# Performance work log

Measured on AMD Instinct MI355X. Metric: run time of the kernel, lower is better.

## Reference

```python
import jax, jax.numpy as jnp
import numpy as np

EPS = 1e-6

def _rmsnorm(x, w):
    var = jnp.mean(x * x, axis=-1, keepdims=True)
    return x * jax.lax.rsqrt(var + EPS) * w

def setup_inputs() -> dict:
    key = jax.random.key(0)
    ks = jax.random.split(key, 10)
    B, S, D = 2, 2048, 1024
    H, E, F = 16, 8, 4096
    std = 0.02
    return {
        "x": jax.random.normal(ks[0], (B, S, D), dtype=jnp.float32),
        "ln1_w": jnp.ones((D,), dtype=jnp.float32),
        "ln2_w": jnp.ones((D,), dtype=jnp.float32),
        "wq": jax.random.normal(ks[1], (D, D), dtype=jnp.float32) * std,
        "wk": jax.random.normal(ks[2], (D, D), dtype=jnp.float32) * std,
        "wv": jax.random.normal(ks[3], (D, D), dtype=jnp.float32) * std,
        "wo": jax.random.normal(ks[4], (D, D), dtype=jnp.float32) * std,
        "wr": jax.random.normal(ks[5], (D, E), dtype=jnp.float32) * std,
        "w1": jax.random.normal(ks[6], (E, D, F), dtype=jnp.float32) * std,
        "w2": jax.random.normal(ks[7], (E, F, D), dtype=jnp.float32) * std,
    }

def reference(x, ln1_w, ln2_w, wq, wk, wv, wo, wr, w1, w2):
    B, S, D = x.shape
    H = 16
    Dh = D // H
    E = wr.shape[1]
    K = 2
    Z_COEF = 0.001

    # --- bidirectional attention sublayer ---
    residual = x
    xn = _rmsnorm(x, ln1_w)
    q = (xn @ wq).reshape(B, S, H, Dh).transpose(0, 2, 1, 3)  # [B,H,S,Dh]
    k = (xn @ wk).reshape(B, S, H, Dh).transpose(0, 2, 1, 3)
    v = (xn @ wv).reshape(B, S, H, Dh).transpose(0, 2, 1, 3)
    scale = 1.0 / jnp.sqrt(jnp.asarray(Dh, dtype=x.dtype))
    scores = jnp.einsum("bhqd,bhkd->bhqk", q, k) * scale  # non-causal
    attn = jax.nn.softmax(scores, axis=-1)
    ctx = jnp.einsum("bhqk,bhkd->bhqd", attn, v)
    attn_out = ctx.transpose(0, 2, 1, 3).reshape(B, S, D) @ wo
    x = residual + attn_out

    # --- MoE sublayer ---
    residual = x
    xn2 = _rmsnorm(x, ln2_w)
    logits = xn2 @ wr                       # [B,S,E]
    probs = jax.nn.softmax(logits, axis=-1)
    topv, topi = jax.lax.top_k(probs, K)    # [B,S,K]
    weights = topv / jnp.sum(topv, axis=-1, keepdims=True)
    onehot = jax.nn.one_hot(topi, E, dtype=x.dtype)          # [B,S,K,E]
    dispatch = jnp.sum(onehot * weights[..., None], axis=-2)  # [B,S,E] combine weights

    # router losses: switch-style load balance + z-loss
    frac_tokens = jnp.mean(jnp.sum(onehot, axis=-2), axis=(0, 1))  # [E]
    frac_probs = jnp.mean(probs, axis=(0, 1))                      # [E]
    aux_loss = E * jnp.sum(frac_tokens * frac_probs) / K
    z = jax.nn.logsumexp(logits, axis=-1)
    router_loss = aux_loss + Z_COEF * jnp.mean(z * z)

    # expert-grouped FFN: dense per expert, masked combine (loop over fixed E)
    expert_out = jnp.zeros_like(xn2)
    for e in range(E):
        h = jax.nn.gelu(xn2 @ w1[e])
        expert_out = expert_out + dispatch[..., e:e + 1] * (h @ w2[e])

    out = residual + expert_out
    return out, router_loss
```

## Files before the change

### kernel.cpp

```cpp
#include <hip/hip_runtime.h>
#include <hip/hip_bf16.h>
#include <math.h>

#define DEV static __device__ __forceinline__

typedef __attribute__((ext_vector_type(8))) short short8;
typedef __attribute__((ext_vector_type(8))) unsigned short ushort8;
typedef __attribute__((ext_vector_type(4))) unsigned short ushort4v;
typedef __attribute__((ext_vector_type(4))) float floatx4;

using bf16 = __hip_bfloat16;

constexpr int Bc = 2, Sc = 2048, Dc = 1024, Hc = 16, DHc = 64, Ec = 8, Fc = 4096;
constexpr int Tc = Bc * Sc;

DEV float b2f(unsigned short u) {
  union { unsigned int i; float f; } c; c.i = ((unsigned int)u) << 16; return c.f;
}
DEV unsigned short f2b(float f) {
  bf16 h = __float2bfloat16(f);
  return *(unsigned short*)&h;
}

DEV floatx4 mfma_bf16(short8 a, short8 b, floatx4 c) {
  return __builtin_amdgcn_mfma_f32_16x16x32_bf16(a, b, c, 0, 0, 0);
}

DEV float gelu_tanh(float x) {
  float z = 0.7978845608028654f * (x + 0.044715f * x * x * x);
  z = fminf(fmaxf(z, -15.f), 15.f);
  float t = __expf(2.f * z);
  return 0.5f * x * (1.f + (t - 1.f) / (t + 1.f));
}

DEV void gemm_core(bf16* As, bf16* Bs,
                   const bf16* __restrict__ A, int lda, int Mvalid, int m0,
                   const float* __restrict__ Bm, int N, int Kdim, int n0,
                   floatx4 (&acc)[4][4]) {
  const int tid = threadIdx.x;
  const int lane = tid & 63;
  const int wave = tid >> 6;
  const int wm = wave & 1, wn = wave >> 1;
  const int l15 = lane & 15, quad = lane >> 4;
  (void)lane;

#pragma unroll
  for (int mi = 0; mi < 4; mi++)
#pragma unroll
    for (int ni = 0; ni < 4; ni++)
#pragma unroll
      for (int r = 0; r < 4; r++) acc[mi][ni][r] = 0.f;

  const int nK = Kdim >> 6;
  for (int kb = 0; kb < nK; kb++) {
    const int k0 = kb << 6;
    __syncthreads();
#pragma unroll
    for (int it = 0; it < 4; it++) {
      int c = tid + it * 256;
      int row = c >> 3, kc = (c & 7) << 3;
      short8 v;
      if (m0 + row < Mvalid) {
        v = *(const short8*)(A + (size_t)(m0 + row) * lda + k0 + kc);
      } else {
#pragma unroll
        for (int j = 0; j < 8; j++) v[j] = 0;
      }
      *(short8*)(As + row * 72 + kc) = v;
    }
#pragma unroll
    for (int it = 0; it < 2; it++) {
      int u = tid + it * 256;
      int kp = u >> 4, cg = u & 15;
      const float* bp = Bm + (size_t)(k0 + 2 * kp) * N + n0 + cg * 8;
      floatx4 r0a = *(const floatx4*)bp;
      floatx4 r0b = *(const floatx4*)(bp + 4);
      floatx4 r1a = *(const floatx4*)(bp + N);
      floatx4 r1b = *(const floatx4*)(bp + N + 4);
#pragma unroll
      for (int j = 0; j < 8; j++) {
        float v0 = (j < 4) ? r0a[j] : r0b[j - 4];
        float v1 = (j < 4) ? r1a[j] : r1b[j - 4];
        int col = cg * 8 + j;
        int elem = col * 72 + ((((kp >> 2) ^ (col >> 3)) & 7) << 3) + ((kp & 3) << 1);
        *(unsigned int*)(Bs + elem) = (unsigned int)f2b(v0) | ((unsigned int)f2b(v1) << 16);
      }
    }
    __syncthreads();
#pragma unroll
    for (int kk = 0; kk < 64; kk += 32) {
      const int gbase = (kk >> 3) & 4;
      short8 af[4], bfr[4];
#pragma unroll
      for (int mi = 0; mi < 4; mi++)
        af[mi] = *(const short8*)(As + (wm * 64 + mi * 16 + l15) * 72 + kk + quad * 8);
#pragma unroll
      for (int ni = 0; ni < 4; ni++) {
        int col = wn * 64 + ni * 16 + l15;
        int g = quad + gbase;
        bfr[ni] = *(const short8*)(Bs + col * 72 + (((g ^ (col >> 3)) & 7) << 3));
      }
#pragma unroll
      for (int mi = 0; mi < 4; mi++)
#pragma unroll
        for (int ni = 0; ni < 4; ni++)
          acc[mi][ni] = mfma_bf16(af[mi], bfr[ni], acc[mi][ni]);
    }
  }
}

#define GEMM_SHARED \
  __shared__ __align__(16) bf16 As[128 * 72]; \
  __shared__ __align__(16) bf16 Bs[128 * 72];
#define LANE_DECODE \
  const int tid = threadIdx.x; const int lane = tid & 63; const int wave = tid >> 6; \
  const int wm = wave & 1, wn = wave >> 1; const int l15 = lane & 15, quad = lane >> 4; \
  (void)tid; (void)lane;

__global__ __launch_bounds__(256) void k_rms(const float* __restrict__ x,
                                             const float* __restrict__ w,
                                             bf16* __restrict__ out,
                                             float* __restrict__ outf) {
  __shared__ float red[4];
  const int tid = threadIdx.x, lane = tid & 63, wave = tid >> 6;
  const size_t base = (size_t)blockIdx.x * Dc + tid * 4;
  floatx4 v = *(const floatx4*)(x + base);
  float ss = v[0] * v[0] + v[1] * v[1] + v[2] * v[2] + v[3] * v[3];
#pragma unroll
  for (int off = 32; off >= 1; off >>= 1) ss += __shfl_xor(ss, off);
  if (lane == 0) red[wave] = ss;
  __syncthreads();
  float tot = red[0] + red[1] + red[2] + red[3];
  float rr = rsqrtf(tot * (1.f / Dc) + 1e-6f);
  floatx4 wv = *(const floatx4*)(w + tid * 4);
  floatx4 res;
#pragma unroll
  for (int j = 0; j < 4; j++) res[j] = v[j] * rr * wv[j];
#pragma unroll
  for (int j = 0; j < 4; j++) out[base + j] = __float2bfloat16(res[j]);
  if (outf) *(floatx4*)(outf + base) = res;
}

__global__ __launch_bounds__(256) void k_gemm_qkv(
    const bf16* __restrict__ xn, const float* __restrict__ wq,
    const float* __restrict__ wk, const float* __restrict__ wv,
    bf16* __restrict__ q, bf16* __restrict__ k, bf16* __restrict__ v) {
  GEMM_SHARED; LANE_DECODE;
  const float* W = blockIdx.z == 0 ? wq : (blockIdx.z == 1 ? wk : wv);
  bf16* out = blockIdx.z == 0 ? q : (blockIdx.z == 1 ? k : v);
  const int m0 = blockIdx.y * 128, n0 = blockIdx.x * 128;
  floatx4 acc[4][4];
  gemm_core(As, Bs, xn, Dc, Tc, m0, W, Dc, Dc, n0, acc);
#pragma unroll
  for (int mi = 0; mi < 4; mi++)
#pragma unroll
    for (int ni = 0; ni < 4; ni++)
#pragma unroll
      for (int r = 0; r < 4; r++) {
        int row = m0 + wm * 64 + mi * 16 + quad * 4 + r;
        int col = n0 + wn * 64 + ni * 16 + l15;
        int b = row >> 11, s = row & 2047, h = col >> 6, dh = col & 63;
        out[((((size_t)b * Hc + h) * Sc + s) << 6) + dh] = __float2bfloat16(acc[mi][ni][r]);
      }
}

__global__ __launch_bounds__(256) void k_gemm_wo(
    const bf16* __restrict__ ctx, const float* __restrict__ wo,
    const float* __restrict__ x, float* __restrict__ x1) {
  GEMM_SHARED; LANE_DECODE;
  const int m0 = blockIdx.y * 128, n0 = blockIdx.x * 128;
  floatx4 acc[4][4];
  gemm_core(As, Bs, ctx, Dc, Tc, m0, wo, Dc, Dc, n0, acc);
#pragma unroll
  for (int mi = 0; mi < 4; mi++)
#pragma unroll
    for (int ni = 0; ni < 4; ni++)
#pragma unroll
      for (int r = 0; r < 4; r++) {
        int row = m0 + wm * 64 + mi * 16 + quad * 4 + r;
        int col = n0 + wn * 64 + ni * 16 + l15;
        size_t idx = (size_t)row * Dc + col;
        x1[idx] = acc[mi][ni][r] + x[idx];
      }
}

__global__ __launch_bounds__(256) void k_attn(
    const bf16* __restrict__ Q, const bf16* __restrict__ K,
    const bf16* __restrict__ V, bf16* __restrict__ ctx) {
  __shared__ __align__(16) bf16 Ks[32 * 72];
  __shared__ __align__(16) bf16 Vs[64 * 40];
  __shared__ __align__(16) bf16 Ps[4 * 16 * 40];
  const int tid = threadIdx.x, lane = tid & 63, wave = tid >> 6;
  const int l15 = lane & 15, quad = lane >> 4;
  const int bh = blockIdx.y;
  const size_t base = (size_t)bh * Sc * DHc;
  const bf16* Qb = Q + base; const bf16* Kb = K + base; const bf16* Vb = V + base;
  const int q0 = blockIdx.x * 64 + wave * 16;
  bf16* Pw = Ps + wave * (16 * 40);

  short8 aq[2];
#pragma unroll
  for (int kk2 = 0; kk2 < 2; kk2++)
    aq[kk2] = *(const short8*)(Qb + (size_t)(q0 + l15) * 64 + kk2 * 32 + quad * 8);

  float m_i[4], l_i[4];
  floatx4 o[4];
#pragma unroll
  for (int r = 0; r < 4; r++) { m_i[r] = -__builtin_inff(); l_i[r] = 0.f; }
#pragma unroll
  for (int n4 = 0; n4 < 4; n4++)
#pragma unroll
    for (int r = 0; r < 4; r++) o[n4][r] = 0.f;

  for (int kt = 0; kt < Sc / 32; kt++) {
    const int kb = kt * 32;
    __syncthreads();
    {
      int row = tid >> 3, kc = (tid & 7) << 3;
      *(short8*)(Ks + row * 72 + kc) = *(const short8*)(Kb + (size_t)(kb + row) * 64 + kc);
    }
    if (tid < 128) {
      int kp = tid >> 3, dg = tid & 7;
      ushort8 a0 = *(const ushort8*)(Vb + (size_t)(kb + 2 * kp) * 64 + dg * 8);
      ushort8 a1 = *(const ushort8*)(Vb + (size_t)(kb + 2 * kp + 1) * 64 + dg * 8);
#pragma unroll
      for (int j = 0; j < 8; j++) {
        int dh = dg * 8 + j;
        int elem = dh * 40 + ((((kp >> 2) ^ (dh >> 3)) & 3) << 3) + ((kp & 3) << 1);
        *(unsigned int*)(Vs + elem) = (unsigned int)a0[j] | ((unsigned int)a1[j] << 16);
      }
    }
    __syncthreads();
    floatx4 sc[2];
#pragma unroll
    for (int ni = 0; ni < 2; ni++) {
#pragma unroll
      for (int r = 0; r < 4; r++) sc[ni][r] = 0.f;
#pragma unroll
      for (int kk2 = 0; kk2 < 2; kk2++) {
        short8 bk = *(const short8*)(Ks + (ni * 16 + l15) * 72 + kk2 * 32 + quad * 8);
        sc[ni] = mfma_bf16(aq[kk2], bk, sc[ni]);
      }
    }
#pragma unroll
    for (int ni = 0; ni < 2; ni++)
#pragma unroll
      for (int r = 0; r < 4; r++) sc[ni][r] *= 0.125f;
    float rmax[4];
#pragma unroll
    for (int r = 0; r < 4; r++) rmax[r] = fmaxf(sc[0][r], sc[1][r]);
#pragma unroll
    for (int off = 1; off < 16; off <<= 1)
#pragma unroll
      for (int r = 0; r < 4; r++) rmax[r] = fmaxf(rmax[r], __shfl_xor(rmax[r], off));
    float alpha[4], rsum[4];
#pragma unroll
    for (int r = 0; r < 4; r++) {
      float nm = fmaxf(m_i[r], rmax[r]);
      alpha[r] = __expf(m_i[r] - nm);
      m_i[r] = nm;
    }
#pragma unroll
    for (int ni = 0; ni < 2; ni++)
#pragma unroll
      for (int r = 0; r < 4; r++) sc[ni][r] = __expf(sc[ni][r] - m_i[r]);
#pragma unroll
    for (int r = 0; r < 4; r++) rsum[r] = sc[0][r] + sc[1][r];
#pragma unroll
    for (int off = 1; off < 16; off <<= 1)
#pragma unroll
      for (int r = 0; r < 4; r++) rsum[r] += __shfl_xor(rsum[r], off);
#pragma unroll
    for (int r = 0; r < 4; r++) l_i[r] = l_i[r] * alpha[r] + rsum[r];
#pragma unroll
    for (int n4 = 0; n4 < 4; n4++)
#pragma unroll
      for (int r = 0; r < 4; r++) o[n4][r] *= alpha[r];
#pragma unroll
    for (int ni = 0; ni < 2; ni++)
#pragma unroll
      for (int r = 0; r < 4; r++)
        Pw[(quad * 4 + r) * 40 + ni * 16 + l15] = __float2bfloat16(sc[ni][r]);
    __syncthreads();
    short8 ap = *(const short8*)(Pw + l15 * 40 + quad * 8);
#pragma unroll
    for (int n4 = 0; n4 < 4; n4++) {
      int dh = n4 * 16 + l15;
      short8 bv = *(const short8*)(Vs + dh * 40 + (((quad ^ (dh >> 3)) & 3) << 3));
      o[n4] = mfma_bf16(ap, bv, o[n4]);
    }
  }
  const int b = bh >> 4, h = bh & 15;
#pragma unroll
  for (int n4 = 0; n4 < 4; n4++)
#pragma unroll
    for (int r = 0; r < 4; r++) {
      int s = q0 + quad * 4 + r;
      int d = h * 64 + n4 * 16 + l15;
      ctx[(size_t)(b * Sc + s) * Dc + d] = __float2bfloat16(o[n4][r] / l_i[r]);
    }
}

__global__ __launch_bounds__(256) void k_router(
    const float* __restrict__ xn2f, const float* __restrict__ wr,
    int* __restrict__ topi, float* __restrict__ topw,
    int* __restrict__ counts, float* __restrict__ sum_probs,
    float* __restrict__ sum_z2) {
  __shared__ float sp[8]; __shared__ float sz[1]; __shared__ int scnt[8];
  const int tid = threadIdx.x, wave = tid >> 6, lane = tid & 63;
  if (tid < 8) { sp[tid] = 0.f; scnt[tid] = 0; }
  if (tid == 0) sz[0] = 0.f;
  __syncthreads();
  const int t = blockIdx.x * 4 + wave;
  float a[8];
#pragma unroll
  for (int e = 0; e < 8; e++) a[e] = 0.f;
  const float* xr = xn2f + (size_t)t * Dc;
#pragma unroll 4
  for (int i = 0; i < 16; i++) {
    int d = lane + i * 64;
    float xv = xr[d];
    floatx4 wa = *(const floatx4*)(wr + d * 8);
    floatx4 wb = *(const floatx4*)(wr + d * 8 + 4);
#pragma unroll
    for (int e = 0; e < 4; e++) a[e] += xv * wa[e];
#pragma unroll
    for (int e = 0; e < 4; e++) a[e + 4] += xv * wb[e];
  }
#pragma unroll
  for (int off = 1; off < 64; off <<= 1)
#pragma unroll
    for (int e = 0; e < 8; e++) a[e] += __shfl_xor(a[e], off);
  float mx = a[0];
#pragma unroll
  for (int e = 1; e < 8; e++) mx = fmaxf(mx, a[e]);
  float pr[8], sum = 0.f;
#pragma unroll
  for (int e = 0; e < 8; e++) { pr[e] = __expf(a[e] - mx); sum += pr[e]; }
  float inv = 1.f / sum;
#pragma unroll
  for (int e = 0; e < 8; e++) pr[e] *= inv;
  float lse = mx + logf(sum);
  int i0 = 0; float p0 = pr[0];
#pragma unroll
  for (int e = 1; e < 8; e++) if (pr[e] > p0) { p0 = pr[e]; i0 = e; }
  int i1 = -1; float p1 = -1.f;
#pragma unroll
  for (int e = 0; e < 8; e++) if (e != i0 && pr[e] > p1) { p1 = pr[e]; i1 = e; }
  float wsum = p0 + p1;
  if (lane == 0) {
    topi[2 * t] = i0; topi[2 * t + 1] = i1;
    topw[2 * t] = p0 / wsum; topw[2 * t + 1] = p1 / wsum;
    atomicAdd(&scnt[i0], 1); atomicAdd(&scnt[i1], 1);
#pragma unroll
    for (int e = 0; e < 8; e++) atomicAdd(&sp[e], pr[e]);
    atomicAdd(&sz[0], lse * lse);
  }
  __syncthreads();
  if (tid < 8) { atomicAdd(&counts[tid], scnt[tid]); atomicAdd(&sum_probs[tid], sp[tid]); }
  if (tid == 0) atomicAdd(sum_z2, sz[0]);
}

__global__ void k_meta(const int* __restrict__ counts, int* __restrict__ offs,
                       const float* __restrict__ sum_probs,
                       const float* __restrict__ sum_z2, float* __restrict__ loss_out) {
  float aux = 0.f;
  offs[0] = 0;
  for (int e = 0; e < 8; e++) {
    offs[e + 1] = offs[e] + counts[e];
    aux += ((float)counts[e] / Tc) * (sum_probs[e] / Tc);
  }
  float loss = (float)Ec * aux * 0.5f + 0.001f * (sum_z2[0] / Tc);
  loss_out[0] = loss;
}

__global__ __launch_bounds__(256) void k_gather(
    const bf16* __restrict__ xn2, const int* __restrict__ topi,
    const int* __restrict__ offs, int* __restrict__ cursors,
    int* __restrict__ rowpos, bf16* __restrict__ Ag) {
  const int tid = threadIdx.x, wave = tid >> 6, lane = tid & 63;
  const int t = blockIdx.x * 4 + wave;
  const int i0 = topi[2 * t], i1 = topi[2 * t + 1];
  int r0 = 0, r1 = 0;
  if (lane == 0) {
    r0 = atomicAdd(&cursors[i0], 1);
    r1 = atomicAdd(&cursors[i1], 1);
    rowpos[2 * t] = r0; rowpos[2 * t + 1] = r1;
  }
  r0 = __shfl(r0, 0); r1 = __shfl(r1, 0);
  const short8* src = (const short8*)(xn2 + (size_t)t * Dc);
  short8 c0 = src[lane], c1 = src[lane + 64];
  short8* d0 = (short8*)(Ag + (size_t)(offs[i0] + r0) * Dc);
  short8* d1 = (short8*)(Ag + (size_t)(offs[i1] + r1) * Dc);
  d0[lane] = c0; d0[lane + 64] = c1;
  d1[lane] = c0; d1[lane + 64] = c1;
}

__global__ __launch_bounds__(256) void k_ffn1(
    const bf16* __restrict__ Ag, const float* __restrict__ w1,
    bf16* __restrict__ Hb, const int* __restrict__ offs) {
  const int e = blockIdx.z;
  const int cnt = offs[e + 1] - offs[e];
  const int m0 = blockIdx.y * 128;
  if (m0 >= cnt) return;
  GEMM_SHARED; LANE_DECODE;
  const int n0 = blockIdx.x * 128;
  const bf16* A = Ag + (size_t)offs[e] * Dc;
  const float* W = w1 + (size_t)e * Dc * Fc;
  bf16* Hp = Hb + (size_t)offs[e] * Fc;
  floatx4 acc[4][4];
  gemm_core(As, Bs, A, Dc, cnt, m0, W, Fc, Dc, n0, acc);
#pragma unroll
  for (int mi = 0; mi < 4; mi++)
#pragma unroll
    for (int ni = 0; ni < 4; ni++)
#pragma unroll
      for (int r = 0; r < 4; r++) {
        int row = m0 + wm * 64 + mi * 16 + quad * 4 + r;
        int col = n0 + wn * 64 + ni * 16 + l15;
        if (row < cnt)
          Hp[(size_t)row * Fc + col] = __float2bfloat16(gelu_tanh(acc[mi][ni][r]));
      }
}

__global__ __launch_bounds__(256) void k_ffn2(
    const bf16* __restrict__ Hb, const float* __restrict__ w2,
    float* __restrict__ Ob, const int* __restrict__ offs) {
  const int e = blockIdx.z;
  const int cnt = offs[e + 1] - offs[e];
  const int m0 = blockIdx.y * 128;
  if (m0 >= cnt) return;
  GEMM_SHARED; LANE_DECODE;
  const int n0 = blockIdx.x * 128;
  const bf16* A = Hb + (size_t)offs[e] * Fc;
  const float* W = w2 + (size_t)e * Fc * Dc;
  float* Op = Ob + (size_t)offs[e] * Dc;
  floatx4 acc[4][4];
  gemm_core(As, Bs, A, Fc, cnt, m0, W, Dc, Fc, n0, acc);
#pragma unroll
  for (int mi = 0; mi < 4; mi++)
#pragma unroll
    for (int ni = 0; ni < 4; ni++)
#pragma unroll
      for (int r = 0; r < 4; r++) {
        int row = m0 + wm * 64 + mi * 16 + quad * 4 + r;
        int col = n0 + wn * 64 + ni * 16 + l15;
        if (row < cnt) Op[(size_t)row * Dc + col] = acc[mi][ni][r];
      }
}

__global__ __launch_bounds__(256) void k_combine(
    const float* __restrict__ x1, const float* __restrict__ Ob,
    const int* __restrict__ topi, const float* __restrict__ topw,
    const int* __restrict__ rowpos, const int* __restrict__ offs,
    float* __restrict__ out) {
  const int t = blockIdx.x, tid = threadIdx.x;
  const int i0 = topi[2 * t], i1 = topi[2 * t + 1];
  const float w0 = topw[2 * t], w1 = topw[2 * t + 1];
  const float* o0 = Ob + (size_t)(offs[i0] + rowpos[2 * t]) * Dc;
  const float* o1 = Ob + (size_t)(offs[i1] + rowpos[2 * t + 1]) * Dc;
  const float* xr = x1 + (size_t)t * Dc;
  floatx4 a = *(const floatx4*)(xr + tid * 4);
  floatx4 b = *(const floatx4*)(o0 + tid * 4);
  floatx4 c = *(const floatx4*)(o1 + tid * 4);
  floatx4 res;
#pragma unroll
  for (int j = 0; j < 4; j++) res[j] = a[j] + w0 * b[j] + w1 * c[j];
  *(floatx4*)(out + (size_t)t * Dc + tid * 4) = res;
}

extern "C" void kernel_launch(void* const* d_in, const int* in_sizes, int n_in,
                              void* d_out, int out_size, void* d_ws, size_t ws_size,
                              hipStream_t stream) {
  (void)in_sizes; (void)n_in; (void)out_size; (void)ws_size;
  const float* x    = (const float*)d_in[0];
  const float* ln1w = (const float*)d_in[1];
  const float* ln2w = (const float*)d_in[2];
  const float* wq   = (const float*)d_in[3];
  const float* wk   = (const float*)d_in[4];
  const float* wv   = (const float*)d_in[5];
  const float* wo   = (const float*)d_in[6];
  const float* wr   = (const float*)d_in[7];
  const float* w1   = (const float*)d_in[8];
  const float* w2   = (const float*)d_in[9];
  float* out = (float*)d_out;

  char* p = (char*)d_ws;
  auto take = [&](size_t bytes) {
    char* r = p; p += (bytes + 255) & ~(size_t)255; return r;
  };
  bf16*  xn   = (bf16*)take((size_t)Tc * Dc * 2);
  bf16*  qb   = (bf16*)take((size_t)Tc * Dc * 2);
  bf16*  kb   = (bf16*)take((size_t)Tc * Dc * 2);
  bf16*  vb   = (bf16*)take((size_t)Tc * Dc * 2);
  bf16*  ctx  = (bf16*)take((size_t)Tc * Dc * 2);
  float* x1   = (float*)take((size_t)Tc * Dc * 4);
  bf16*  xn2  = (bf16*)take((size_t)Tc * Dc * 2);
  float* xn2f = (float*)take((size_t)Tc * Dc * 4);
  bf16*  Ag   = (bf16*)take((size_t)2 * Tc * Dc * 2);
  bf16*  Hb   = (bf16*)take((size_t)2 * Tc * Fc * 2);
  float* Ob   = (float*)take((size_t)2 * Tc * Dc * 4);
  int*   counts    = (int*)take(512);
  int*   cursors   = counts + 8;
  float* sum_probs = (float*)(counts + 16);
  float* sum_z2    = sum_probs + 8;
  int*   offs      = (int*)take(256);
  int*   topi      = (int*)take((size_t)2 * Tc * 4);
  float* topw      = (float*)take((size_t)2 * Tc * 4);
  int*   rowpos    = (int*)take((size_t)2 * Tc * 4);

  hipMemsetAsync(counts, 0, 512, stream);

  k_rms<<<Tc, 256, 0, stream>>>(x, ln1w, xn, nullptr);
  k_gemm_qkv<<<dim3(Dc / 128, Tc / 128, 3), 256, 0, stream>>>(xn, wq, wk, wv, qb, kb, vb);
  k_attn<<<dim3(Sc / 64, Bc * Hc), 256, 0, stream>>>(qb, kb, vb, ctx);
  k_gemm_wo<<<dim3(Dc / 128, Tc / 128), 256, 0, stream>>>(ctx, wo, x, x1);
  k_rms<<<Tc, 256, 0, stream>>>(x1, ln2w, xn2, xn2f);
  k_router<<<Tc / 4, 256, 0, stream>>>(xn2f, wr, topi, topw, counts, sum_probs, sum_z2);
  k_meta<<<1, 1, 0, stream>>>(counts, offs, sum_probs, sum_z2, out + (size_t)Tc * Dc);
  k_gather<<<Tc / 4, 256, 0, stream>>>(xn2, topi, offs, cursors, rowpos, Ag);
  k_ffn1<<<dim3(Fc / 128, Tc / 128, Ec), 256, 0, stream>>>(Ag, w1, Hb, offs);
  k_ffn2<<<dim3(Dc / 128, Tc / 128, Ec), 256, 0, stream>>>(Hb, w2, Ob, offs);
  k_combine<<<Tc, 256, 0, stream>>>(x1, Ob, topi, topw, rowpos, offs, out);
}
```

Measured before the change: 1.028 ms.

## Pre-transpose weights to bf16 and stream GEMM tiles via direct global-to-LDS loads

Adds transpose kernels that convert every fp32 weight matrix (attention projections, w1, w2) into K-contiguous bf16 copies in workspace on each call. The shared GEMM core then loads both operands with global_load_lds 16-byte copies straight into unpadded LDS tiles. This removes the per-tile fp32 loads, bf16 conversion and swizzled scalar LDS stores. The cost is an extra full pass over the large expert weights each call. The unpadded LDS layout may cause bank conflicts, and the row-validity guard is dropped, so A-tile loads can read past each expert's rows (outputs are still masked).

```diff
diff --git a/kernel.cpp b/kernel.cpp
--- a/kernel.cpp
+++ b/kernel.cpp
@@ -1,26 +1,18 @@
 #include <hip/hip_runtime.h>
 #include <hip/hip_bf16.h>
 #include <math.h>
+#include <stdint.h>
 
 #define DEV static __device__ __forceinline__
 
 typedef __attribute__((ext_vector_type(8))) short short8;
 typedef __attribute__((ext_vector_type(8))) unsigned short ushort8;
-typedef __attribute__((ext_vector_type(4))) unsigned short ushort4v;
 typedef __attribute__((ext_vector_type(4))) float floatx4;
 
 using bf16 = __hip_bfloat16;
 
 constexpr int Bc = 2, Sc = 2048, Dc = 1024, Hc = 16, DHc = 64, Ec = 8, Fc = 4096;
 constexpr int Tc = Bc * Sc;
-
-DEV float b2f(unsigned short u) {
-  union { unsigned int i; float f; } c; c.i = ((unsigned int)u) << 16; return c.f;
-}
-DEV unsigned short f2b(float f) {
-  bf16 h = __float2bfloat16(f);
-  return *(unsigned short*)&h;
-}
 
 DEV floatx4 mfma_bf16(short8 a, short8 b, floatx4 c) {
   return __builtin_amdgcn_mfma_f32_16x16x32_bf16(a, b, c, 0, 0, 0);
@@ -33,16 +25,62 @@
   return 0.5f * x * (1.f + (t - 1.f) / (t + 1.f));
 }
 
+DEV void gl16(const void* g, void* l) {
+  __builtin_amdgcn_global_load_lds(
+      reinterpret_cast<const __attribute__((address_space(1))) void*>(
+          reinterpret_cast<uintptr_t>(g)),
+      reinterpret_cast<__attribute__((address_space(3))) void*>(
+          reinterpret_cast<uintptr_t>(l)),
+      16, 0, 0);
+}
+
+DEV void tr_tile(const float* __restrict__ W, bf16* __restrict__ Wt,
+                 int K, int N, bf16 (*Ts)[72]) {
+  const int n0 = blockIdx.x * 64, k0 = blockIdx.y * 64;
+  const int tid = threadIdx.x;
+#pragma unroll
+  for (int it = 0; it < 4; it++) {
+    int u = tid + it * 256;
+    int r = u >> 4, c4 = (u & 15) << 2;
+    floatx4 v = *(const floatx4*)(W + (size_t)(k0 + r) * N + n0 + c4);
+#pragma unroll
+    for (int j = 0; j < 4; j++) Ts[c4 + j][r] = __float2bfloat16(v[j]);
+  }
+  __syncthreads();
+#pragma unroll
+  for (int it = 0; it < 2; it++) {
+    int u = tid + it * 256;
+    int rn = u >> 3, kc = (u & 7) << 3;
+    *(short8*)(Wt + (size_t)(n0 + rn) * K + k0 + kc) = *(const short8*)(&Ts[rn][kc]);
+  }
+}
+
+__global__ __launch_bounds__(256) void k_wt(const float* __restrict__ W,
+                                            bf16* __restrict__ Wt, int K, int N) {
+  __shared__ __align__(16) bf16 Ts[64][72];
+  const size_t mb = (size_t)blockIdx.z * K * N;
+  tr_tile(W + mb, Wt + mb, K, N, Ts);
+}
+
+__global__ __launch_bounds__(256) void k_wt4(
+    const float* __restrict__ a, const float* __restrict__ b,
+    const float* __restrict__ c, const float* __restrict__ d,
+    bf16* __restrict__ o) {
+  __shared__ __align__(16) bf16 Ts[64][72];
+  const int z = blockIdx.z;
+  const float* W = z == 0 ? a : (z == 1 ? b : (z == 2 ? c : d));
+  tr_tile(W, o + (size_t)z * Dc * Dc, Dc, Dc, Ts);
+}
+
 DEV void gemm_core(bf16* As, bf16* Bs,
-                   const bf16* __restrict__ A, int lda, int Mvalid, int m0,
-                   const float* __restrict__ Bm, int N, int Kdim, int n0,
-                   floatx4 (&acc)[4][4]) {
+                   const bf16* __restrict__ A, int lda, int m0,
+                   const bf16* __restrict__ Bt, int ldb, int n0,
+                   int Kdim, floatx4 (&acc)[4][4]) {
   const int tid = threadIdx.x;
   const int lane = tid & 63;
   const int wave = tid >> 6;
   const int wm = wave & 1, wn = wave >> 1;
   const int l15 = lane & 15, quad = lane >> 4;
-  (void)lane;
 
 #pragma unroll
   for (int mi = 0; mi < 4; mi++)
@@ -51,55 +89,29 @@
 #pragma unroll
       for (int r = 0; r < 4; r++) acc[mi][ni][r] = 0.f;
 
+  const int arow = tid >> 3;
+  const int akc = (tid & 7) << 3;
   const int nK = Kdim >> 6;
   for (int kb = 0; kb < nK; kb++) {
     const int k0 = kb << 6;
     __syncthreads();
 #pragma unroll
     for (int it = 0; it < 4; it++) {
-      int c = tid + it * 256;
-      int row = c >> 3, kc = (c & 7) << 3;
-      short8 v;
-      if (m0 + row < Mvalid) {
-        v = *(const short8*)(A + (size_t)(m0 + row) * lda + k0 + kc);
-      } else {
-#pragma unroll
-        for (int j = 0; j < 8; j++) v[j] = 0;
-      }
-      *(short8*)(As + row * 72 + kc) = v;
-    }
-#pragma unroll
-    for (int it = 0; it < 2; it++) {
-      int u = tid + it * 256;
-      int kp = u >> 4, cg = u & 15;
-      const float* bp = Bm + (size_t)(k0 + 2 * kp) * N + n0 + cg * 8;
-      floatx4 r0a = *(const floatx4*)bp;
-      floatx4 r0b = *(const floatx4*)(bp + 4);
-      floatx4 r1a = *(const floatx4*)(bp + N);
-      floatx4 r1b = *(const floatx4*)(bp + N + 4);
-#pragma unroll
-      for (int j = 0; j < 8; j++) {
-        float v0 = (j < 4) ? r0a[j] : r0b[j - 4];
-        float v1 = (j < 4) ? r1a[j] : r1b[j - 4];
-        int col = cg * 8 + j;
-        int elem = col * 72 + ((((kp >> 2) ^ (col >> 3)) & 7) << 3) + ((kp & 3) << 1);
-        *(unsigned int*)(Bs + elem) = (unsigned int)f2b(v0) | ((unsigned int)f2b(v1) << 16);
-      }
+      const int row = arow + it * 32;
+      const int lbase = (it * 256 + wave * 64) * 8;
+      gl16(A + (size_t)(m0 + row) * lda + k0 + akc, As + lbase);
+      gl16(Bt + (size_t)(n0 + row) * ldb + k0 + akc, Bs + lbase);
     }
     __syncthreads();
 #pragma unroll
     for (int kk = 0; kk < 64; kk += 32) {
-      const int gbase = (kk >> 3) & 4;
       short8 af[4], bfr[4];
 #pragma unroll
       for (int mi = 0; mi < 4; mi++)
-        af[mi] = *(const short8*)(As + (wm * 64 + mi * 16 + l15) * 72 + kk + quad * 8);
-#pragma unroll
-      for (int ni = 0; ni < 4; ni++) {
-        int col = wn * 64 + ni * 16 + l15;
-        int g = quad + gbase;
-        bfr[ni] = *(const short8*)(Bs + col * 72 + (((g ^ (col >> 3)) & 7) << 3));
-      }
+        af[mi] = *(const short8*)(As + (wm * 64 + mi * 16 + l15) * 64 + kk + quad * 8);
+#pragma unroll
+      for (int ni = 0; ni < 4; ni++)
+        bfr[ni] = *(const short8*)(Bs + (wn * 64 + ni * 16 + l15) * 64 + kk + quad * 8);
 #pragma unroll
       for (int mi = 0; mi < 4; mi++)
 #pragma unroll
@@ -110,8 +122,8 @@
 }
 
 #define GEMM_SHARED \
-  __shared__ __align__(16) bf16 As[128 * 72]; \
-  __shared__ __align__(16) bf16 Bs[128 * 72];
+  __shared__ __align__(16) bf16 As[128 * 64]; \
+  __shared__ __align__(16) bf16 Bs[128 * 64];
 #define LANE_DECODE \
   const int tid = threadIdx.x; const int lane = tid & 63; const int wave = tid >> 6; \
   const int wm = wave & 1, wn = wave >> 1; const int l15 = lane & 15, quad = lane >> 4; \
@@ -142,15 +154,14 @@
 }
 
 __global__ __launch_bounds__(256) void k_gemm_qkv(
-    const bf16* __restrict__ xn, const float* __restrict__ wq,
-    const float* __restrict__ wk, const float* __restrict__ wv,
+    const bf16* __restrict__ xn, const bf16* __restrict__ wt,
     bf16* __restrict__ q, bf16* __restrict__ k, bf16* __restrict__ v) {
   GEMM_SHARED; LANE_DECODE;
-  const float* W = blockIdx.z == 0 ? wq : (blockIdx.z == 1 ? wk : wv);
+  const bf16* W = wt + (size_t)blockIdx.z * Dc * Dc;
   bf16* out = blockIdx.z == 0 ? q : (blockIdx.z == 1 ? k : v);
   const int m0 = blockIdx.y * 128, n0 = blockIdx.x * 128;
   floatx4 acc[4][4];
-  gemm_core(As, Bs, xn, Dc, Tc, m0, W, Dc, Dc, n0, acc);
+  gemm_core(As, Bs, xn, Dc, m0, W, Dc, n0, Dc, acc);
 #pragma unroll
   for (int mi = 0; mi < 4; mi++)
 #pragma unroll
@@ -165,12 +176,12 @@
 }
 
 __global__ __launch_bounds__(256) void k_gemm_wo(
-    const bf16* __restrict__ ctx, const float* __restrict__ wo,
+    const bf16* __restrict__ ctx, const bf16* __restrict__ wot,
     const float* __restrict__ x, float* __restrict__ x1) {
   GEMM_SHARED; LANE_DECODE;
   const int m0 = blockIdx.y * 128, n0 = blockIdx.x * 128;
   floatx4 acc[4][4];
-  gemm_core(As, Bs, ctx, Dc, Tc, m0, wo, Dc, Dc, n0, acc);
+  gemm_core(As, Bs, ctx, Dc, m0, wot, Dc, n0, Dc, acc);
 #pragma unroll
   for (int mi = 0; mi < 4; mi++)
 #pragma unroll
@@ -397,7 +408,7 @@
 }
 
 __global__ __launch_bounds__(256) void k_ffn1(
-    const bf16* __restrict__ Ag, const float* __restrict__ w1,
+    const bf16* __restrict__ Ag, const bf16* __restrict__ w1t,
     bf16* __restrict__ Hb, const int* __restrict__ offs) {
   const int e = blockIdx.z;
   const int cnt = offs[e + 1] - offs[e];
@@ -406,10 +417,10 @@
   GEMM_SHARED; LANE_DECODE;
   const int n0 = blockIdx.x * 128;
   const bf16* A = Ag + (size_t)offs[e] * Dc;
-  const float* W = w1 + (size_t)e * Dc * Fc;
+  const bf16* W = w1t + (size_t)e * Dc * Fc;
   bf16* Hp = Hb + (size_t)offs[e] * Fc;
   floatx4 acc[4][4];
-  gemm_core(As, Bs, A, Dc, cnt, m0, W, Fc, Dc, n0, acc);
+  gemm_core(As, Bs, A, Dc, m0, W, Dc, n0, Dc, acc);
 #pragma unroll
   for (int mi = 0; mi < 4; mi++)
 #pragma unroll
@@ -424,7 +435,7 @@
 }
 
 __global__ __launch_bounds__(256) void k_ffn2(
-    const bf16* __restrict__ Hb, const float* __restrict__ w2,
+    const bf16* __restrict__ Hb, const bf16* __restrict__ w2t,
     float* __restrict__ Ob, const int* __restrict__ offs) {
   const int e = blockIdx.z;
   const int cnt = offs[e + 1] - offs[e];
@@ -433,10 +444,10 @@
   GEMM_SHARED; LANE_DECODE;
   const int n0 = blockIdx.x * 128;
   const bf16* A = Hb + (size_t)offs[e] * Fc;
-  const float* W = w2 + (size_t)e * Fc * Dc;
+  const bf16* W = w2t + (size_t)e * Fc * Dc;
   float* Op = Ob + (size_t)offs[e] * Dc;
   floatx4 acc[4][4];
-  gemm_core(As, Bs, A, Fc, cnt, m0, W, Dc, Fc, n0, acc);
+  gemm_core(As, Bs, A, Fc, m0, W, Fc, n0, Fc, acc);
 #pragma unroll
   for (int mi = 0; mi < 4; mi++)
 #pragma unroll
@@ -500,6 +511,8 @@
   bf16*  Ag   = (bf16*)take((size_t)2 * Tc * Dc * 2);
   bf16*  Hb   = (bf16*)take((size_t)2 * Tc * Fc * 2);
   float* Ob   = (float*)take((size_t)2 * Tc * Dc * 4);
+  bf16*  wtqkvo = (bf16*)take((size_t)4 * Dc * Dc * 2);
+  bf16*  wtbig  = (bf16*)take((size_t)Ec * (size_t)Dc * Fc * 2);
   int*   counts    = (int*)take(512);
   int*   cursors   = counts + 8;
   float* sum_probs = (float*)(counts + 16);
@@ -511,15 +524,19 @@
 
   hipMemsetAsync(counts, 0, 512, stream);
 
+  k_wt4<<<dim3(Dc / 64, Dc / 64, 4), 256, 0, stream>>>(wq, wk, wv, wo, wtqkvo);
+  k_wt<<<dim3(Fc / 64, Dc / 64, Ec), 256, 0, stream>>>(w1, wtbig, Dc, Fc);
+
   k_rms<<<Tc, 256, 0, stream>>>(x, ln1w, xn, nullptr);
-  k_gemm_qkv<<<dim3(Dc / 128, Tc / 128, 3), 256, 0, stream>>>(xn, wq, wk, wv, qb, kb, vb);
+  k_gemm_qkv<<<dim3(Dc / 128, Tc / 128, 3), 256, 0, stream>>>(xn, wtqkvo, qb, kb, vb);
   k_attn<<<dim3(Sc / 64, Bc * Hc), 256, 0, stream>>>(qb, kb, vb, ctx);
-  k_gemm_wo<<<dim3(Dc / 128, Tc / 128), 256, 0, stream>>>(ctx, wo, x, x1);
+  k_gemm_wo<<<dim3(Dc / 128, Tc / 128), 256, 0, stream>>>(ctx, wtqkvo + (size_t)3 * Dc * Dc, x, x1);
   k_rms<<<Tc, 256, 0, stream>>>(x1, ln2w, xn2, xn2f);
   k_router<<<Tc / 4, 256, 0, stream>>>(xn2f, wr, topi, topw, counts, sum_probs, sum_z2);
   k_meta<<<1, 1, 0, stream>>>(counts, offs, sum_probs, sum_z2, out + (size_t)Tc * Dc);
   k_gather<<<Tc / 4, 256, 0, stream>>>(xn2, topi, offs, cursors, rowpos, Ag);
-  k_ffn1<<<dim3(Fc / 128, Tc / 128, Ec), 256, 0, stream>>>(Ag, w1, Hb, offs);
-  k_ffn2<<<dim3(Dc / 128, Tc / 128, Ec), 256, 0, stream>>>(Hb, w2, Ob, offs);
+  k_ffn1<<<dim3(Fc / 128, Tc / 128, Ec), 256, 0, stream>>>(Ag, wtbig, Hb, offs);
+  k_wt<<<dim3(Dc / 64, Fc / 64, Ec), 256, 0, stream>>>(w2, wtbig, Fc, Dc);
+  k_ffn2<<<dim3(Dc / 128, Tc / 128, Ec), 256, 0, stream>>>(Hb, wtbig, Ob, offs);
   k_combine<<<Tc, 256, 0, stream>>>(x1, Ob, topi, topw, rowpos, offs, out);
 }
```

Result: slower. 1.082 ms (+5.2%).
